# Kernel optimization log

Hardware: AMD Instinct MI355X
Metric: run time of the kernel (lower is better)

## Reference

```python
import jax, jax.numpy as jnp
import numpy as np

N_H, N_O, D = 5000, 15000, 1024
E_HH, E_OO, E_HO = 20000, 40000, 40000


def setup_inputs() -> dict:
    key = jax.random.key(0)
    ks = jax.random.split(key, 20)
    N = N_H + N_O
    w = lambda k, shp: jax.random.normal(k, shp, dtype=jnp.float32) * 0.02
    inp = {
        'n_f': jax.random.normal(ks[0], (N, D), dtype=jnp.float32),
        'src_hh': jax.random.randint(ks[1], (E_HH,), 0, N_H),
        'dst_hh': jax.random.randint(ks[2], (E_HH,), 0, N_H),
        'src_oo': jax.random.randint(ks[3], (E_OO,), 0, N_O) + N_H,
        'dst_oo': jax.random.randint(ks[4], (E_OO,), 0, N_O) + N_H,
        'src_ho': jax.random.randint(ks[5], (E_HO,), 0, N_H),
        'dst_ho': jax.random.randint(ks[6], (E_HO,), 0, N_O) + N_H,
        'W_hh': w(ks[7], (2 * D, D)), 'b_hh': jnp.zeros((D,), jnp.float32),
        'W_oo': w(ks[8], (2 * D, D)), 'b_oo': jnp.zeros((D,), jnp.float32),
        'W_ho': w(ks[9], (2 * D, D)), 'b_ho': jnp.zeros((D,), jnp.float32),
        'W_att': w(ks[10], (D, 1)), 'b_att': jnp.zeros((1,), jnp.float32),
        'W_hn': w(ks[11], (2 * D, D)), 'b_hn': jnp.zeros((D,), jnp.float32),
        'W_on': w(ks[12], (2 * D, D)), 'b_on': jnp.zeros((D,), jnp.float32),
    }
    return inp


def reference(n_f, src_hh, dst_hh, src_oo, dst_oo, src_ho, dst_ho,
              W_hh, b_hh, W_oo, b_oo, W_ho, b_ho, W_att, b_att,
              W_hn, b_hn, W_on, b_on):
    N = n_f.shape[0]

    def edge_mlp(src, dst, W, b):
        # gather -> concat -> Linear -> ReLU  (H_H/O_O/H_O EdgeApplyModule)
        feat = jnp.concatenate([n_f[src], n_f[dst]], axis=1)  # [E, 2D]
        return jax.nn.relu(feat @ W + b)                       # [E, D]

    e_f = jnp.concatenate([
        edge_mlp(src_hh, dst_hh, W_hh, b_hh),
        edge_mlp(src_oo, dst_oo, W_oo, b_oo),
        edge_mlp(src_ho, dst_ho, W_ho, b_ho),
    ], axis=0)                                                 # [E, D]
    src = jnp.concatenate([src_hh, src_oo, src_ho])
    dst = jnp.concatenate([dst_hh, dst_oo, dst_ho])

    # E_AttentionModule: per-edge scalar attention logit
    a = (e_f @ W_att + b_att)[:, 0]                            # [E]

    # update_all: per-destination softmax over incoming edges (mailbox softmax)
    seg_max = jax.ops.segment_max(a, dst, num_segments=N)
    seg_max = jnp.where(jnp.isfinite(seg_max), seg_max, 0.0)
    ex = jnp.exp(a - seg_max[dst])
    denom = jax.ops.segment_sum(ex, dst, num_segments=N)
    alpha = ex / jnp.where(denom[dst] == 0, 1.0, denom[dst])   # [E]
    z = jax.ops.segment_sum(alpha[:, None] * n_f[src], dst, num_segments=N)  # [N, D]

    # Node apply: concat(n_f, z_f) -> Linear -> ReLU, separate h/o MLPs
    new_h = jax.nn.relu(jnp.concatenate([n_f[:N_H], z[:N_H]], axis=1) @ W_hn + b_hn)
    new_o = jax.nn.relu(jnp.concatenate([n_f[N_H:], z[N_H:]], axis=1) @ W_on + b_on)
    return jnp.concatenate([new_h, new_o], axis=0)             # [N, D] new_n_f
```

## Files before the change

### kernel.cpp

```cpp
#include <hip/hip_runtime.h>

#define N_H   5000
#define N_O   15000
#define N_TOT 20000
#define DD    1024
#define E_HH  20000
#define E_OO  40000
#define E_HO  40000
#define E_TOT 100000
#define CAP   128

typedef unsigned short u16;
typedef unsigned int u32;
typedef __attribute__((ext_vector_type(8))) short short8;
typedef __attribute__((ext_vector_type(4))) float f32x4;
typedef const __attribute__((address_space(1))) u32 gas_u32;
typedef __attribute__((address_space(3))) u32 las_u32;

__device__ __forceinline__ float bf2f(u16 u) {
    union { unsigned int i; float f; } v; v.i = ((unsigned int)u) << 16; return v.f;
}
__device__ __forceinline__ u16 f2bf(float f) {
    union { float f; unsigned int i; } v; v.f = f;
    unsigned int u = v.i;
    return (u16)((u + 0x7FFFu + ((u >> 16) & 1u)) >> 16);
}

#define CAST_NB 10000
#define CAT_NB  391
#define ZERO_NB 79
#define TW_NB   10240
struct TW  { const float* W; u16* dT; u16* dB; int ld; };
struct TW5 { TW t[5]; };
__global__ void cast_cat_tw(const float* __restrict__ in, u16* __restrict__ out,
                            const int* __restrict__ shh, const int* __restrict__ dhh,
                            const int* __restrict__ soo, const int* __restrict__ doo,
                            const int* __restrict__ sho, const int* __restrict__ dho,
                            int* __restrict__ src_all, int* __restrict__ dst_all,
                            int* __restrict__ cursor, TW5 p) {
    __shared__ float tile[32][33];
    int b = blockIdx.x;
    if (b < CAST_NB) {
        size_t i = ((size_t)b * 256 + threadIdx.x) * 8;
        float4 a = *(const float4*)(in + i);
        float4 c = *(const float4*)(in + i + 4);
        u16 o[8] = {f2bf(a.x), f2bf(a.y), f2bf(a.z), f2bf(a.w),
                    f2bf(c.x), f2bf(c.y), f2bf(c.z), f2bf(c.w)};
        *(uint4*)(out + i) = *(const uint4*)o;
        return;
    }
    if (b < CAST_NB + CAT_NB) {
        int e = (b - CAST_NB) * 256 + threadIdx.x;
        if (e >= E_TOT) return;
        int s, d;
        if (e < E_HH)              { s = shh[e];               d = dhh[e]; }
        else if (e < E_HH + E_OO)  { s = soo[e - E_HH];        d = doo[e - E_HH]; }
        else                       { s = sho[e - E_HH - E_OO]; d = dho[e - E_HH - E_OO]; }
        src_all[e] = s; dst_all[e] = d;
        return;
    }
    if (b < CAST_NB + CAT_NB + ZERO_NB) {
        int i = (b - CAST_NB - CAT_NB) * 256 + threadIdx.x;
        if (i < N_TOT) cursor[i] = 0;
        return;
    }
    int tb = b - CAST_NB - CAT_NB - ZERO_NB;
    int z = tb >> 10;
    int rem = tb & 1023;
    int bk = rem & 31, bn = rem >> 5;
    TW tw = p.t[z >> 1];
    int half = z & 1;
    int tx = threadIdx.x & 31, ty = threadIdx.x >> 5;
#pragma unroll
    for (int yy = 0; yy < 4; yy++) {
        int k = half * 1024 + bk * 32 + ty + yy * 8;
        int n = bn * 32 + tx;
        tile[ty + yy * 8][tx] = tw.W[(size_t)k * 1024 + n];
    }
    __syncthreads();
    u16* dst = half ? tw.dB : tw.dT;
#pragma unroll
    for (int yy = 0; yy < 4; yy++) {
        int n = bn * 32 + ty + yy * 8;
        int k = bk * 32 + tx;
        dst[(size_t)n * tw.ld + k] = f2bf(tile[tx][ty + yy * 8]);
    }
}

#define PROJ_NBM_H 40
#define PROJ_NBM_O 118
#define PROJ_NBN   24
#define PROJ_GEMM_NB ((PROJ_NBM_H + PROJ_NBM_O) * PROJ_NBN)
#define FILL_NB 391
__launch_bounds__(256)
__global__ void gemm_proj(const u16* __restrict__ Ah, const u16* __restrict__ Ao,
                          const u16* __restrict__ Bth, const u16* __restrict__ Bto,
                          u16* __restrict__ Ch, u16* __restrict__ Co,
                          const int* __restrict__ dst_all, int* __restrict__ cursor,
                          int* __restrict__ edge_ids) {
    __shared__ u16 smem[2][128][64];
    int bid = blockIdx.x;
    if (bid >= PROJ_GEMM_NB) {
        int e = (bid - PROJ_GEMM_NB) * 256 + threadIdx.x;
        if (e < E_TOT) {
            int d = dst_all[e];
            int pos = atomicAdd(&cursor[d], 1);
            if (pos < CAP) edge_ids[(size_t)d * CAP + pos] = e;
        }
        return;
    }
    const u16* A; const u16* Bt; u16* C; int M;
    if (bid < PROJ_NBM_H * PROJ_NBN) { A = Ah; Bt = Bth; C = Ch; M = N_H; }
    else { bid -= PROJ_NBM_H * PROJ_NBN; A = Ao; Bt = Bto; C = Co; M = N_O; }
    int bm = bid / PROJ_NBN, bn = bid % PROJ_NBN;
    int t = threadIdx.x;
    int wave = t >> 6, lane = t & 63;
    int wr = wave >> 1, wc = wave & 1;
    int lm = lane & 15, q = lane >> 4;
    f32x4 acc[4][4] = {};
    int srow = lane >> 3;
    int scol = ((lane & 7) ^ srow) * 8;

    for (int k0 = 0; k0 < 1024; k0 += 64) {
#pragma unroll
        for (int it = 0; it < 4; it++) {
            int chunk = wave * 4 + it;
            int row = chunk * 8 + srow;
            int gr = bm * 128 + row; if (gr >= M) gr = M - 1;
            __builtin_amdgcn_global_load_lds((gas_u32*)(A + (size_t)gr * 1024 + k0 + scol),
                                             (las_u32*)&smem[0][chunk * 8][0], 16, 0, 0);
            __builtin_amdgcn_global_load_lds((gas_u32*)(Bt + (size_t)(bn * 128 + row) * 1024 + k0 + scol),
                                             (las_u32*)&smem[1][chunk * 8][0], 16, 0, 0);
        }
        __syncthreads();
#pragma unroll
        for (int ks = 0; ks < 64; ks += 32) {
            short8 af[4], bfr[4];
            int pc = (((ks >> 3) + q) ^ (lm & 7)) * 8;
#pragma unroll
            for (int i = 0; i < 4; i++)
                af[i] = *(const short8*)&smem[0][wr * 64 + i * 16 + lm][pc];
#pragma unroll
            for (int j = 0; j < 4; j++)
                bfr[j] = *(const short8*)&smem[1][wc * 64 + j * 16 + lm][pc];
#pragma unroll
            for (int i = 0; i < 4; i++)
#pragma unroll
                for (int j = 0; j < 4; j++)
                    acc[i][j] = __builtin_amdgcn_mfma_f32_16x16x32_bf16(af[i], bfr[j], acc[i][j], 0, 0, 0);
        }
        __syncthreads();
    }
    u16* sc = &smem[0][0][0];
#pragma unroll
    for (int i = 0; i < 4; i++)
#pragma unroll
        for (int j = 0; j < 4; j++)
#pragma unroll
            for (int r = 0; r < 4; r++)
                sc[(wr * 64 + i * 16 + q * 4 + r) * 128 + (wc * 64 + j * 16 + lm)] =
                    f2bf(acc[i][j][r]);
    __syncthreads();
#pragma unroll
    for (int it = 0; it < 8; it++) {
        int flat = it * 256 + t;
        int r = flat >> 4, cs = (flat & 15) * 8;
        int grow = bm * 128 + r;
        if (grow < M)
            *(uint4*)&C[(size_t)grow * 3072 + bn * 128 + cs] = *(const uint4*)&sc[r * 128 + cs];
    }
}

#define NODE_NBM_H 40
#define NODE_NBM_O 118
#define NODE_NBN   8
__launch_bounds__(256)
__global__ void gemm_node(const u16* __restrict__ nf_h, const u16* __restrict__ nf_o,
                          const u16* __restrict__ z_h, const u16* __restrict__ z_o,
                          const u16* __restrict__ Bthn, const u16* __restrict__ Bton,
                          const float* __restrict__ b_hn, const float* __restrict__ b_on,
                          float* __restrict__ out_h, float* __restrict__ out_o) {
    __shared__ u16 smem[2][128][64];
    int bid = (blockIdx.x & 7) * ((NODE_NBM_H + NODE_NBM_O) * NODE_NBN / 8)
            + (blockIdx.x >> 3);
    const u16 *A0, *A1, *Bt; const float* bias; float* C; int M;
    if (bid < NODE_NBM_H * NODE_NBN) {
        A0 = nf_h; A1 = z_h; Bt = Bthn; bias = b_hn; C = out_h; M = N_H;
    } else {
        bid -= NODE_NBM_H * NODE_NBN;
        A0 = nf_o; A1 = z_o; Bt = Bton; bias = b_on; C = out_o; M = N_O;
    }
    int bm = bid / NODE_NBN, bn = bid % NODE_NBN;
    int t = threadIdx.x;
    int wave = t >> 6, lane = t & 63;
    int wr = wave >> 1, wc = wave & 1;
    int lm = lane & 15, q = lane >> 4;
    f32x4 acc[4][4] = {};
    int srow = lane >> 3;
    int scol = ((lane & 7) ^ srow) * 8;

    for (int half = 0; half < 2; half++) {
        const u16* Asrc = half ? A1 : A0;
        const u16* Bth = Bt + half * 1024;
        for (int k0 = 0; k0 < 1024; k0 += 64) {
#pragma unroll
            for (int it = 0; it < 4; it++) {
                int chunk = wave * 4 + it;
                int row = chunk * 8 + srow;
                int gr = bm * 128 + row; if (gr >= M) gr = M - 1;
                __builtin_amdgcn_global_load_lds((gas_u32*)(Asrc + (size_t)gr * 1024 + k0 + scol),
                                                 (las_u32*)&smem[0][chunk * 8][0], 16, 0, 0);
                __builtin_amdgcn_global_load_lds((gas_u32*)(Bth + (size_t)(bn * 128 + row) * 2048 + k0 + scol),
                                                 (las_u32*)&smem[1][chunk * 8][0], 16, 0, 0);
            }
            __syncthreads();
#pragma unroll
            for (int ks = 0; ks < 64; ks += 32) {
                short8 af[4], bfr[4];
                int pc = (((ks >> 3) + q) ^ (lm & 7)) * 8;
#pragma unroll
                for (int i = 0; i < 4; i++)
                    af[i] = *(const short8*)&smem[0][wr * 64 + i * 16 + lm][pc];
#pragma unroll
                for (int j = 0; j < 4; j++)
                    bfr[j] = *(const short8*)&smem[1][wc * 64 + j * 16 + lm][pc];
#pragma unroll
                for (int i = 0; i < 4; i++)
#pragma unroll
                    for (int j = 0; j < 4; j++)
                        acc[i][j] = __builtin_amdgcn_mfma_f32_16x16x32_bf16(af[i], bfr[j], acc[i][j], 0, 0, 0);
            }
            __syncthreads();
        }
    }
    float* sf = (float*)&smem[0][0][0];
#pragma unroll
    for (int p = 0; p < 2; p++) {
        if (p) __syncthreads();
        if (wr == p) {
#pragma unroll
            for (int j = 0; j < 4; j++) {
                int col = wc * 64 + j * 16 + lm;
                float bv = bias[bn * 128 + col];
#pragma unroll
                for (int i = 0; i < 4; i++)
#pragma unroll
                    for (int r = 0; r < 4; r++)
                        sf[(i * 16 + q * 4 + r) * 128 + col] =
                            fmaxf(acc[i][j][r] + bv, 0.0f);
            }
        }
        __syncthreads();
#pragma unroll
        for (int it = 0; it < 8; it++) {
            int c = it * 256 + t;
            int rl = c >> 5, k4 = c & 31;
            int grow = bm * 128 + p * 64 + rl;
            if (grow < M)
                *(float4*)&C[(size_t)grow * 1024 + bn * 128 + k4 * 4] =
                    *(const float4*)&sf[rl * 128 + k4 * 4];
        }
    }
}

__global__ void edge_att(const u16* __restrict__ proj_h, const u16* __restrict__ proj_o,
                         const float* __restrict__ b_hh, const float* __restrict__ b_oo,
                         const float* __restrict__ b_ho,
                         const float* __restrict__ W_att, const float* __restrict__ b_att,
                         const int* __restrict__ src_all, const int* __restrict__ dst_all,
                         float* __restrict__ a_out) {
    int wave = threadIdx.x >> 6, lane = threadIdx.x & 63;
    int e0 = blockIdx.x * 64 + wave * 16;
    if (e0 >= E_TOT) return;
    const float* bsel = (e0 < E_HH) ? b_hh : (e0 < E_HH + E_OO ? b_oo : b_ho);
    float ww[16], bb[16];
#pragma unroll
    for (int i = 0; i < 16; i++) { ww[i] = W_att[lane * 16 + i]; bb[i] = bsel[lane * 16 + i]; }
    float batt = b_att[0];
    for (int k = 0; k < 16; k++) {
        int e = e0 + k;
        int s = src_all[e], d = dst_all[e];
        const u16 *u, *v;
        if (e < E_HH) {
            u = proj_h + (size_t)s * 3072;
            v = proj_h + (size_t)d * 3072 + 1024;
        } else if (e < E_HH + E_OO) {
            u = proj_o + (size_t)(s - N_H) * 3072;
            v = proj_o + (size_t)(d - N_H) * 3072 + 1024;
        } else {
            u = proj_h + (size_t)s * 3072 + 2048;
            v = proj_o + (size_t)(d - N_H) * 3072 + 2048;
        }
        int off = lane * 16;
        uint4 u0 = *(const uint4*)(u + off), u1 = *(const uint4*)(u + off + 8);
        uint4 v0 = *(const uint4*)(v + off), v1 = *(const uint4*)(v + off + 8);
        const u16* pu0 = (const u16*)&u0; const u16* pu1 = (const u16*)&u1;
        const u16* pv0 = (const u16*)&v0; const u16* pv1 = (const u16*)&v1;
        float acc = 0.f;
#pragma unroll
        for (int i = 0; i < 8; i++) {
            float tv = bf2f(pu0[i]) + bf2f(pv0[i]) + bb[i];
            acc += fmaxf(tv, 0.f) * ww[i];
        }
#pragma unroll
        for (int i = 0; i < 8; i++) {
            float tv = bf2f(pu1[i]) + bf2f(pv1[i]) + bb[8 + i];
            acc += fmaxf(tv, 0.f) * ww[8 + i];
        }
#pragma unroll
        for (int o = 32; o > 0; o >>= 1) acc += __shfl_down(acc, o);
        if (lane == 0) a_out[e] = acc + batt;
    }
}

__launch_bounds__(256)
__global__ void soft_z_w(const float* __restrict__ a, const int* __restrict__ cursor,
                         const int* __restrict__ edge_ids, const int* __restrict__ src_all,
                         const u16* __restrict__ nf, u16* __restrict__ z) {
    int wave = threadIdx.x >> 6, lane = threadIdx.x & 63;
    int node = blockIdx.x * 4 + wave;
    if (node >= N_TOT) return;
    int deg = cursor[node]; if (deg > CAP) deg = CAP;
    const int* elist = edge_ids + (size_t)node * CAP;
    float m = -1e30f, ssum = 0.f;
    for (int i = lane; i < deg; i += 64) {
        float av = a[elist[i]];
        if (av > m) { ssum *= __expf(m - av); m = av; }
        ssum += __expf(av - m);
    }
#pragma unroll
    for (int o = 32; o > 0; o >>= 1) {
        float m2 = __shfl_xor(m, o);
        float s2 = __shfl_xor(ssum, o);
        float mn = fmaxf(m, m2);
        ssum = ssum * __expf(m - mn) + s2 * __expf(m2 - mn);
        m = mn;
    }
    float inv = (ssum > 0.f) ? 1.0f / ssum : 0.f;
    float av16[16] = {};
    int base = lane * 16;
    for (int i = 0; i < deg; i++) {
        int eid = elist[i];
        float al = __expf(a[eid] - m) * inv;
        const u16* row = nf + (size_t)src_all[eid] * DD + base;
        uint4 p0 = *(const uint4*)row;
        uint4 p1 = *(const uint4*)(row + 8);
        const u16* pp0 = (const u16*)&p0;
        const u16* pp1 = (const u16*)&p1;
#pragma unroll
        for (int j = 0; j < 8; j++) av16[j]     += al * bf2f(pp0[j]);
#pragma unroll
        for (int j = 0; j < 8; j++) av16[8 + j] += al * bf2f(pp1[j]);
    }
    u16 ov[16];
#pragma unroll
    for (int j = 0; j < 16; j++) ov[j] = f2bf(av16[j]);
    const uint4* po = (const uint4*)ov;
    *(uint4*)(z + (size_t)node * DD + base)     = po[0];
    *(uint4*)(z + (size_t)node * DD + base + 8) = po[1];
}

extern "C" void kernel_launch(void* const* d_in, const int* in_sizes, int n_in,
                              void* d_out, int out_size, void* d_ws, size_t ws_size,
                              hipStream_t stream) {
    const float* nf   = (const float*)d_in[0];
    const int* shh    = (const int*)d_in[1];
    const int* dhh    = (const int*)d_in[2];
    const int* soo    = (const int*)d_in[3];
    const int* doo    = (const int*)d_in[4];
    const int* sho    = (const int*)d_in[5];
    const int* dho    = (const int*)d_in[6];
    const float* W_hh = (const float*)d_in[7];
    const float* b_hh = (const float*)d_in[8];
    const float* W_oo = (const float*)d_in[9];
    const float* b_oo = (const float*)d_in[10];
    const float* W_ho = (const float*)d_in[11];
    const float* b_ho = (const float*)d_in[12];
    const float* W_att= (const float*)d_in[13];
    const float* b_att= (const float*)d_in[14];
    const float* W_hn = (const float*)d_in[15];
    const float* b_hn = (const float*)d_in[16];
    const float* W_on = (const float*)d_in[17];
    const float* b_on = (const float*)d_in[18];
    float* out = (float*)d_out;

    char* ws = (char*)d_ws;
    size_t off = 0;
    auto alloc = [&](size_t bytes) -> char* {
        char* p = ws + off;
        off += (bytes + 255) & ~(size_t)255;
        return p;
    };
    u16* nf_bf = (u16*)alloc((size_t)N_TOT * DD * 2);
    u16* Bt_h  = (u16*)alloc((size_t)3072 * 1024 * 2);
    u16* Bt_o  = (u16*)alloc((size_t)3072 * 1024 * 2);
    u16* Bt_hn = (u16*)alloc((size_t)1024 * 2048 * 2);
    u16* Bt_on = (u16*)alloc((size_t)1024 * 2048 * 2);
    u16* proj_h = (u16*)alloc((size_t)N_H * 3072 * 2);
    u16* proj_o = (u16*)alloc((size_t)N_O * 3072 * 2);
    u16* z_bf   = proj_h;
    float* a_log  = (float*)alloc(E_TOT * 4);
    int* src_all  = (int*)alloc(E_TOT * 4);
    int* dst_all  = (int*)alloc(E_TOT * 4);
    int* deg      = (int*)alloc(2 * N_TOT * 4);
    int* cursor   = deg + N_TOT;
    int* edge_ids = (int*)alloc((size_t)N_TOT * CAP * 4);
    (void)ws_size; (void)in_sizes; (void)n_in; (void)out_size;

    TW5 tws;
    tws.t[0] = {W_hh, Bt_h,                       Bt_h + (size_t)1024 * 1024, 1024};
    tws.t[1] = {W_oo, Bt_o,                       Bt_o + (size_t)1024 * 1024, 1024};
    tws.t[2] = {W_ho, Bt_h + (size_t)2048 * 1024, Bt_o + (size_t)2048 * 1024, 1024};
    tws.t[3] = {W_hn, Bt_hn,                      Bt_hn + 1024,               2048};
    tws.t[4] = {W_on, Bt_on,                      Bt_on + 1024,               2048};
    cast_cat_tw<<<CAST_NB + CAT_NB + ZERO_NB + TW_NB, 256, 0, stream>>>(
        nf, nf_bf, shh, dhh, soo, doo, sho, dho, src_all, dst_all, cursor, tws);

    const u16* nf_bf_o = nf_bf + (size_t)N_H * DD;
    gemm_proj<<<PROJ_GEMM_NB + FILL_NB, 256, 0, stream>>>(
        nf_bf, nf_bf_o, Bt_h, Bt_o, proj_h, proj_o, dst_all, cursor, edge_ids);

    edge_att<<<(E_TOT + 63) / 64, 256, 0, stream>>>(proj_h, proj_o, b_hh, b_oo, b_ho,
                                                    W_att, b_att, src_all, dst_all, a_log);

    soft_z_w<<<N_TOT / 4, 256, 0, stream>>>(a_log, cursor, edge_ids, src_all, nf_bf, z_bf);

    gemm_node<<<(NODE_NBM_H + NODE_NBM_O) * NODE_NBN, 256, 0, stream>>>(
        nf_bf, nf_bf_o, z_bf, z_bf + (size_t)N_H * DD, Bt_hn, Bt_on,
        b_hn, b_on, out, out + (size_t)N_H * DD);
}
```

Baseline: 554.4 us.

## Fuse edge attention logits into per-destination online-softmax aggregation kernel

Removes the separate edge_att kernel and computes each edge's attention logit inside the per-destination-node aggregation wave, using an online softmax that rescales the running z accumulator whenever the max grows. The destination-side projection plus bias is loaded once per node and reused across all incoming edges, and the logit buffer round trip and one launch are dropped. In exchange the per-edge work is serialized inside each node's wave with extra shuffles and rescale multiplies. z now gets its own workspace buffer because proj_h is still read while z is written.

```diff
diff --git a/kernel.cpp b/kernel.cpp
--- a/kernel.cpp
+++ b/kernel.cpp
@@ -263,101 +263,102 @@
     }
 }
 
-__global__ void edge_att(const u16* __restrict__ proj_h, const u16* __restrict__ proj_o,
-                         const float* __restrict__ b_hh, const float* __restrict__ b_oo,
-                         const float* __restrict__ b_ho,
-                         const float* __restrict__ W_att, const float* __restrict__ b_att,
-                         const int* __restrict__ src_all, const int* __restrict__ dst_all,
-                         float* __restrict__ a_out) {
-    int wave = threadIdx.x >> 6, lane = threadIdx.x & 63;
-    int e0 = blockIdx.x * 64 + wave * 16;
-    if (e0 >= E_TOT) return;
-    const float* bsel = (e0 < E_HH) ? b_hh : (e0 < E_HH + E_OO ? b_oo : b_ho);
-    float ww[16], bb[16];
-#pragma unroll
-    for (int i = 0; i < 16; i++) { ww[i] = W_att[lane * 16 + i]; bb[i] = bsel[lane * 16 + i]; }
-    float batt = b_att[0];
-    for (int k = 0; k < 16; k++) {
-        int e = e0 + k;
-        int s = src_all[e], d = dst_all[e];
-        const u16 *u, *v;
-        if (e < E_HH) {
-            u = proj_h + (size_t)s * 3072;
-            v = proj_h + (size_t)d * 3072 + 1024;
-        } else if (e < E_HH + E_OO) {
-            u = proj_o + (size_t)(s - N_H) * 3072;
-            v = proj_o + (size_t)(d - N_H) * 3072 + 1024;
-        } else {
-            u = proj_h + (size_t)s * 3072 + 2048;
-            v = proj_o + (size_t)(d - N_H) * 3072 + 2048;
-        }
-        int off = lane * 16;
-        uint4 u0 = *(const uint4*)(u + off), u1 = *(const uint4*)(u + off + 8);
-        uint4 v0 = *(const uint4*)(v + off), v1 = *(const uint4*)(v + off + 8);
-        const u16* pu0 = (const u16*)&u0; const u16* pu1 = (const u16*)&u1;
-        const u16* pv0 = (const u16*)&v0; const u16* pv1 = (const u16*)&v1;
-        float acc = 0.f;
-#pragma unroll
-        for (int i = 0; i < 8; i++) {
-            float tv = bf2f(pu0[i]) + bf2f(pv0[i]) + bb[i];
-            acc += fmaxf(tv, 0.f) * ww[i];
-        }
-#pragma unroll
-        for (int i = 0; i < 8; i++) {
-            float tv = bf2f(pu1[i]) + bf2f(pv1[i]) + bb[8 + i];
-            acc += fmaxf(tv, 0.f) * ww[8 + i];
-        }
-#pragma unroll
-        for (int o = 32; o > 0; o >>= 1) acc += __shfl_down(acc, o);
-        if (lane == 0) a_out[e] = acc + batt;
-    }
-}
-
 __launch_bounds__(256)
-__global__ void soft_z_w(const float* __restrict__ a, const int* __restrict__ cursor,
-                         const int* __restrict__ edge_ids, const int* __restrict__ src_all,
-                         const u16* __restrict__ nf, u16* __restrict__ z) {
+__global__ void att_soft_z(const int* __restrict__ cursor, const int* __restrict__ edge_ids,
+                           const int* __restrict__ src_all,
+                           const u16* __restrict__ proj_h, const u16* __restrict__ proj_o,
+                           const float* __restrict__ b_hh, const float* __restrict__ b_oo,
+                           const float* __restrict__ b_ho,
+                           const float* __restrict__ W_att, const float* __restrict__ b_att,
+                           const u16* __restrict__ nf, u16* __restrict__ z) {
     int wave = threadIdx.x >> 6, lane = threadIdx.x & 63;
     int node = blockIdx.x * 4 + wave;
     if (node >= N_TOT) return;
     int deg = cursor[node]; if (deg > CAP) deg = CAP;
     const int* elist = edge_ids + (size_t)node * CAP;
+    int isH = node < N_H;
+    int off = lane * 16;
+
+    float ww[16];
+#pragma unroll
+    for (int i = 0; i < 16; i++) ww[i] = W_att[off + i];
+    const float* b0 = isH ? b_hh : b_oo;
+    const u16* v0src = isH ? proj_h + (size_t)node * 3072 + 1024
+                           : proj_o + (size_t)(node - N_H) * 3072 + 1024;
+    uint4 va0 = *(const uint4*)(v0src + off), va1 = *(const uint4*)(v0src + off + 8);
+    const u16* pa0 = (const u16*)&va0; const u16* pa1 = (const u16*)&va1;
+    float vf0[16], vf1[16];
+#pragma unroll
+    for (int j = 0; j < 8; j++) {
+        vf0[j]     = bf2f(pa0[j]) + b0[off + j];
+        vf0[8 + j] = bf2f(pa1[j]) + b0[off + 8 + j];
+    }
+    if (!isH) {
+        const u16* v1src = proj_o + (size_t)(node - N_H) * 3072 + 2048;
+        uint4 vb0 = *(const uint4*)(v1src + off), vb1 = *(const uint4*)(v1src + off + 8);
+        const u16* pb0 = (const u16*)&vb0; const u16* pb1 = (const u16*)&vb1;
+#pragma unroll
+        for (int j = 0; j < 8; j++) {
+            vf1[j]     = bf2f(pb0[j]) + b_ho[off + j];
+            vf1[8 + j] = bf2f(pb1[j]) + b_ho[off + 8 + j];
+        }
+    } else {
+#pragma unroll
+        for (int j = 0; j < 16; j++) vf1[j] = 0.f;
+    }
+    float batt = b_att[0];
+
     float m = -1e30f, ssum = 0.f;
-    for (int i = lane; i < deg; i += 64) {
-        float av = a[elist[i]];
-        if (av > m) { ssum *= __expf(m - av); m = av; }
-        ssum += __expf(av - m);
-    }
-#pragma unroll
-    for (int o = 32; o > 0; o >>= 1) {
-        float m2 = __shfl_xor(m, o);
-        float s2 = __shfl_xor(ssum, o);
-        float mn = fmaxf(m, m2);
-        ssum = ssum * __expf(m - mn) + s2 * __expf(m2 - mn);
-        m = mn;
-    }
-    float inv = (ssum > 0.f) ? 1.0f / ssum : 0.f;
     float av16[16] = {};
-    int base = lane * 16;
     for (int i = 0; i < deg; i++) {
         int eid = elist[i];
-        float al = __expf(a[eid] - m) * inv;
-        const u16* row = nf + (size_t)src_all[eid] * DD + base;
-        uint4 p0 = *(const uint4*)row;
-        uint4 p1 = *(const uint4*)(row + 8);
-        const u16* pp0 = (const u16*)&p0;
-        const u16* pp1 = (const u16*)&p1;
-#pragma unroll
-        for (int j = 0; j < 8; j++) av16[j]     += al * bf2f(pp0[j]);
-#pragma unroll
-        for (int j = 0; j < 8; j++) av16[8 + j] += al * bf2f(pp1[j]);
-    }
+        int s = src_all[eid];
+        const u16* u; int typ1 = 0;
+        if (eid < E_HH)             { u = proj_h + (size_t)s * 3072; }
+        else if (eid < E_HH + E_OO) { u = proj_o + (size_t)(s - N_H) * 3072; }
+        else                        { u = proj_h + (size_t)s * 3072 + 2048; typ1 = 1; }
+        uint4 u0 = *(const uint4*)(u + off), u1 = *(const uint4*)(u + off + 8);
+        const u16* nrow = nf + (size_t)s * DD + off;
+        uint4 p0 = *(const uint4*)nrow, p1 = *(const uint4*)(nrow + 8);
+        const u16* pu0 = (const u16*)&u0; const u16* pu1 = (const u16*)&u1;
+        const u16* pp0 = (const u16*)&p0; const u16* pp1 = (const u16*)&p1;
+        float acc = 0.f;
+#pragma unroll
+        for (int j = 0; j < 8; j++) {
+            float tv = bf2f(pu0[j]) + (typ1 ? vf1[j] : vf0[j]);
+            acc += fmaxf(tv, 0.f) * ww[j];
+        }
+#pragma unroll
+        for (int j = 0; j < 8; j++) {
+            float tv = bf2f(pu1[j]) + (typ1 ? vf1[8 + j] : vf0[8 + j]);
+            acc += fmaxf(tv, 0.f) * ww[8 + j];
+        }
+#pragma unroll
+        for (int o = 32; o > 0; o >>= 1) acc += __shfl_xor(acc, o);
+        float l = acc + batt;
+        float pw;
+        if (l > m) {
+            float sc = __expf(m - l);
+            ssum *= sc;
+#pragma unroll
+            for (int j = 0; j < 16; j++) av16[j] *= sc;
+            m = l; pw = 1.0f;
+        } else {
+            pw = __expf(l - m);
+        }
+        ssum += pw;
+#pragma unroll
+        for (int j = 0; j < 8; j++) av16[j]     += pw * bf2f(pp0[j]);
+#pragma unroll
+        for (int j = 0; j < 8; j++) av16[8 + j] += pw * bf2f(pp1[j]);
+    }
+    float inv = (ssum > 0.f) ? 1.0f / ssum : 0.f;
     u16 ov[16];
 #pragma unroll
-    for (int j = 0; j < 16; j++) ov[j] = f2bf(av16[j]);
+    for (int j = 0; j < 16; j++) ov[j] = f2bf(av16[j] * inv);
     const uint4* po = (const uint4*)ov;
-    *(uint4*)(z + (size_t)node * DD + base)     = po[0];
-    *(uint4*)(z + (size_t)node * DD + base + 8) = po[1];
+    *(uint4*)(z + (size_t)node * DD + off)     = po[0];
+    *(uint4*)(z + (size_t)node * DD + off + 8) = po[1];
 }
 
 extern "C" void kernel_launch(void* const* d_in, const int* in_sizes, int n_in,
@@ -398,8 +399,7 @@
     u16* Bt_on = (u16*)alloc((size_t)1024 * 2048 * 2);
     u16* proj_h = (u16*)alloc((size_t)N_H * 3072 * 2);
     u16* proj_o = (u16*)alloc((size_t)N_O * 3072 * 2);
-    u16* z_bf   = proj_h;
-    float* a_log  = (float*)alloc(E_TOT * 4);
+    u16* z_bf  = (u16*)alloc((size_t)N_TOT * DD * 2);
     int* src_all  = (int*)alloc(E_TOT * 4);
     int* dst_all  = (int*)alloc(E_TOT * 4);
     int* deg      = (int*)alloc(2 * N_TOT * 4);
@@ -420,10 +420,9 @@
     gemm_proj<<<PROJ_GEMM_NB + FILL_NB, 256, 0, stream>>>(
         nf_bf, nf_bf_o, Bt_h, Bt_o, proj_h, proj_o, dst_all, cursor, edge_ids);
 
-    edge_att<<<(E_TOT + 63) / 64, 256, 0, stream>>>(proj_h, proj_o, b_hh, b_oo, b_ho,
-                                                    W_att, b_att, src_all, dst_all, a_log);
-
-    soft_z_w<<<N_TOT / 4, 256, 0, stream>>>(a_log, cursor, edge_ids, src_all, nf_bf, z_bf);
+    att_soft_z<<<N_TOT / 4, 256, 0, stream>>>(cursor, edge_ids, src_all,
+                                              proj_h, proj_o, b_hh, b_oo, b_ho,
+                                              W_att, b_att, nf_bf, z_bf);
 
     gemm_node<<<(NODE_NBM_H + NODE_NBM_O) * NODE_NBN, 256, 0, stream>>>(
         nf_bf, nf_bf_o, z_bf, z_bf + (size_t)N_H * DD, Bt_hn, Bt_on,
```

After: 614.5 us. 10.8% more time.
